# Kernel optimization log

Measured on AMD Instinct MI355X. Metric: run time of the kernel, lower is better.

Reference implementation:

```python
import math
import jax, jax.numpy as jnp
import numpy as np

NUM_HEADS = 16

def _rotate_half(t):
    t1, t2 = jnp.split(t, 2, axis=-1)
    return jnp.concatenate([-t2, t1], axis=-1)

def _apply_rope(t, cos, sin):
    # t: [B, H, S, D]; cos/sin: [S, D] broadcast over batch and heads
    c = cos[None, None, :, :]
    s = sin[None, None, :, :]
    return t * c + _rotate_half(t) * s

def setup_inputs() -> dict:
    key = jax.random.key(0)
    k1, k2, k3, k4, k5 = jax.random.split(key, 5)
    B, S, E, D = 4, 2048, 1024, 1024 // NUM_HEADS
    x = jax.random.normal(k1, (B, S, E), dtype=jnp.float32)
    cos = jax.random.uniform(k2, (S, D), dtype=jnp.float32)
    sin = jax.random.uniform(k3, (S, D), dtype=jnp.float32)
    W_qkv = jax.random.normal(k4, (3 * E, E), dtype=jnp.float32) * (1.0 / math.sqrt(E))
    W_out = jax.random.normal(k5, (E, E), dtype=jnp.float32) * (1.0 / math.sqrt(E))
    return {"x": x, "cos": cos, "sin": sin, "W_qkv": W_qkv, "W_out": W_out}

def reference(x, cos, sin, W_qkv, W_out):
    B, S, E = x.shape
    H = NUM_HEADS
    D = E // H
    # fused QKV projection (torch Linear: y = x @ W^T)
    qkv = jnp.einsum('bse,fe->bsf', x, W_qkv)
    qkv = qkv.reshape(B, S, 3, H, D).transpose(2, 0, 3, 1, 4)  # [3, B, H, S, D]
    q, k, v = qkv[0], qkv[1], qkv[2]
    q = _apply_rope(q, cos, sin)
    k = _apply_rope(k, cos, sin)
    # naive fp32 attention: full [B,H,S,S] score matrix, stable softmax
    scale = 1.0 / math.sqrt(D)
    qf = q.astype(jnp.float32)
    kf = k.astype(jnp.float32)
    vf = v.astype(jnp.float32)
    scores = jnp.einsum('bhqd,bhkd->bhqk', qf, kf) * scale
    attn = jax.nn.softmax(scores, axis=-1)
    o = jnp.einsum('bhqk,bhkd->bhqd', attn, vf).astype(x.dtype)
    o = o.transpose(0, 2, 1, 3).reshape(B, S, E)
    return jnp.einsum('bse,fe->bsf', o, W_out)
```

## Files before the change

kernel.cpp:

```cpp
#include <hip/hip_runtime.h>
#include <hip/hip_bf16.h>

using bf16 = __hip_bfloat16;
typedef __attribute__((ext_vector_type(4))) float f32x4;
typedef __attribute__((ext_vector_type(16))) float f32x16;
typedef short s16x8 __attribute__((ext_vector_type(8)));
typedef unsigned short u16x8 __attribute__((ext_vector_type(8)));

__device__ __forceinline__ unsigned short f2b(float f) {
  bf16 h = __float2bfloat16(f);
  return __builtin_bit_cast(unsigned short, h);
}
__device__ __forceinline__ unsigned cvt_pk_bf16(float lo, float hi) {
  unsigned r;
  asm volatile("v_cvt_pk_bf16_f32 %0, %1, %2" : "=v"(r) : "v"(lo), "v"(hi));
  return r;
}
__device__ __forceinline__ void pl32_swap(unsigned& a, unsigned& b) {
  asm volatile("v_permlane32_swap_b32 %0, %1" : "+v"(a), "+v"(b));
}
__device__ __forceinline__ float fast_exp2(float x) {
#if __has_builtin(__builtin_amdgcn_exp2f)
  return __builtin_amdgcn_exp2f(x);
#else
  return exp2f(x);
#endif
}

__device__ __forceinline__ void async_copy16(const void* g, void* lds) {
  __builtin_amdgcn_global_load_lds(
      (const __attribute__((address_space(1))) void*)g,
      (__attribute__((address_space(3))) void*)lds, 16, 0, 0);
}

__global__ __launch_bounds__(256) void cvt_f32_to_bf16(const float* __restrict__ in,
                                                       ushort* __restrict__ out) {
  long i = ((long)blockIdx.x * 256 + threadIdx.x) * 8;
  float4 a = *(const float4*)(in + i);
  float4 b = *(const float4*)(in + i + 4);
  u16x8 o;
  o[0] = f2b(a.x); o[1] = f2b(a.y); o[2] = f2b(a.z); o[3] = f2b(a.w);
  o[4] = f2b(b.x); o[5] = f2b(b.y); o[6] = f2b(b.z); o[7] = f2b(b.w);
  *(u16x8*)(out + i) = o;
}

__global__ __launch_bounds__(256) void transpose_v(const bf16* __restrict__ qkv,
                                                   ushort* __restrict__ vtg) {
  const int pair = blockIdx.y;
  const int b = pair >> 4, h = pair & 15;
  const int st = blockIdx.x * 64;
  const int tid = threadIdx.x;
  __shared__ ushort T[64][68];
  const ushort* src = (const ushort*)qkv + (long)(b * 2048 + st) * 3072 + 2048 + h * 64;
#pragma unroll
  for (int i = 0; i < 4; ++i) {
    int c2 = tid + i * 256;
    int row = c2 >> 4;
    int d4 = (c2 & 15) * 4;
    *(ushort4*)&T[row][d4] = *(const ushort4*)(src + (long)row * 3072 + d4);
  }
  __syncthreads();
#pragma unroll
  for (int i = 0; i < 4; ++i) {
    int c2 = tid + i * 256;
    int d = c2 >> 4;
    int s4 = (c2 & 15) * 4;
    ushort4 w;
    w.x = T[s4][d]; w.y = T[s4 + 1][d]; w.z = T[s4 + 2][d]; w.w = T[s4 + 3][d];
    *(ushort4*)(vtg + (long)pair * 131072 + (long)d * 2048 + st + s4) = w;
  }
}

__device__ __forceinline__ void storeC(float* p, float v) { *p = v; }
__device__ __forceinline__ void storeC(bf16* p, float v) { *p = __float2bfloat16(v); }

template <typename CT, bool ROPE>
__global__ __launch_bounds__(256) void gemm_bt(const bf16* __restrict__ A,
                                               const bf16* __restrict__ B,
                                               CT* __restrict__ C,
                                               int M, int N, int K,
                                               const float* __restrict__ cosT,
                                               const float* __restrict__ sinT) {
  __shared__ bf16 As[2][128 * 64];
  __shared__ bf16 Bs[2][128 * 64];
  const int tid = threadIdx.x;
  const int lane = tid & 63;
  const int wid = tid >> 6;

  const int nwg = gridDim.x * gridDim.y;
  const int orig = blockIdx.y * gridDim.x + blockIdx.x;
  const int wgid = (orig & 7) * (nwg >> 3) + (orig >> 3);
  const int bx = wgid % gridDim.x;
  const int by = wgid / gridDim.x;

  const int tm = by * 128;
  const int tn = bx * 128;
  const int wr = wid >> 1, wc = wid & 1;
  const int srow = tid >> 3;
  const int scolb = (tid & 7) * 16;
  const int sscolb = scolb ^ ((srow & 7) << 4);

  f32x4 acc[4][4] = {};

  const bf16* Abase = A + (long)(tm + srow) * K + (sscolb >> 1);
  const bf16* Bbase = B + (long)(tn + srow) * K + (sscolb >> 1);

  const int lr = lane & 15;
  const int g = lane >> 4;
  const int sw = (lr & 7) << 4;

  auto stage = [&](int k0, int bb) {
#pragma unroll
    for (int i = 0; i < 4; ++i) {
      async_copy16(Abase + (long)i * 32 * K + k0, (char*)As[bb] + wid * 1024 + i * 4096);
      async_copy16(Bbase + (long)i * 32 * K + k0, (char*)Bs[bb] + wid * 1024 + i * 4096);
    }
  };

  const int nk = K >> 6;
  stage(0, 0);
  stage(64, 1);

  for (int kt = 0; kt < nk; ++kt) {
    const int cur = kt & 1;
    if (kt + 1 < nk) asm volatile("s_waitcnt vmcnt(8)" ::: "memory");
    else             asm volatile("s_waitcnt vmcnt(0)" ::: "memory");
    __builtin_amdgcn_s_barrier();
    __builtin_amdgcn_sched_barrier(0);

#pragma unroll
    for (int ks = 0; ks < 2; ++ks) {
      s16x8 af[4], bff[4];
#pragma unroll
      for (int m = 0; m < 4; ++m) {
        int row = wr * 64 + m * 16 + lr;
        af[m] = *(const s16x8*)((const char*)&As[cur][0] + row * 128 +
                                ((ks * 64 + g * 16) ^ sw));
      }
#pragma unroll
      for (int n = 0; n < 4; ++n) {
        int row = wc * 64 + n * 16 + lr;
        bff[n] = *(const s16x8*)((const char*)&Bs[cur][0] + row * 128 +
                                 ((ks * 64 + g * 16) ^ sw));
      }
#pragma unroll
      for (int m = 0; m < 4; ++m)
#pragma unroll
        for (int n = 0; n < 4; ++n)
          acc[m][n] = __builtin_amdgcn_mfma_f32_16x16x32_bf16(af[m], bff[n], acc[m][n], 0, 0, 0);
    }

    __builtin_amdgcn_s_barrier();
    __builtin_amdgcn_sched_barrier(0);
    if (kt + 2 < nk) stage((kt + 2) << 6, cur);
  }

  const int cc = lane & 15;
  const int cr = (lane >> 4) * 4;
  const int wcol = tn + wc * 64;

  if (ROPE && wcol < 2048) {
    const float sc = (wcol < 1024) ? 0.18033688011112042f : 1.0f;
#pragma unroll
    for (int m = 0; m < 4; ++m)
#pragma unroll
      for (int n = 0; n < 2; ++n) {
        long row0 = tm + wr * 64 + m * 16 + cr;
        long col = wcol + n * 16 + cc;
        int d = n * 16 + cc;
#pragma unroll
        for (int r = 0; r < 4; ++r) {
          int s = (int)((row0 + r) & 2047);
          float lo = acc[m][n][r], hi = acc[m][n + 2][r];
          float c0 = cosT[s * 64 + d], s0v = sinT[s * 64 + d];
          float c1 = cosT[s * 64 + d + 32], s1v = sinT[s * 64 + d + 32];
          storeC(&C[(row0 + r) * (long)N + col], (lo * c0 - hi * s0v) * sc);
          storeC(&C[(row0 + r) * (long)N + col + 32], (hi * c1 + lo * s1v) * sc);
        }
      }
  } else {
#pragma unroll
    for (int m = 0; m < 4; ++m)
#pragma unroll
      for (int n = 0; n < 4; ++n) {
        long row0 = tm + wr * 64 + m * 16 + cr;
        long col = wcol + n * 16 + cc;
#pragma unroll
        for (int r = 0; r < 4; ++r)
          storeC(&C[(row0 + r) * (long)N + col], acc[m][n][r]);
      }
  }
}

__global__ __launch_bounds__(256, 4) void attn_kernel(const bf16* __restrict__ qkv,
                                                      const ushort* __restrict__ vtg,
                                                      ushort* __restrict__ o) {
  const int bid = blockIdx.x;
  const int xcd = bid & 7;
  const int w = bid >> 3;
  const int pair = xcd * 8 + (w >> 4);
  const int qtile = w & 15;
  const int b = pair >> 4, h = pair & 15;
  const int q0 = qtile * 128;
  const int tid = threadIdx.x, lane = tid & 63, wid = tid >> 6;

  const bf16* Qb = qkv + (long)b * 2048 * 3072 + h * 64;
  const bf16* Kb = Qb + 1024;
  const ushort* Vg = vtg + (long)pair * 131072;

  __shared__ bf16 Ks[2][64 * 64];
  __shared__ bf16 Vs[2][64 * 64];

  const int ql = lane & 31;
  const int hi = lane >> 5;
  const int sw = (ql & 7) << 4;

  s16x8 qa[4];
  {
    const bf16* qrow = Qb + (long)(q0 + wid * 32 + ql) * 3072 + hi * 8;
#pragma unroll
    for (int ds = 0; ds < 4; ++ds)
      qa[ds] = *(const s16x8*)(qrow + ds * 16);
  }

  f32x16 oacc[2] = {};
  float lrow = 0.f;

  auto stage = [&](int kt, int bb) {
#pragma unroll
    for (int i = 0; i < 2; ++i) {
      int c = tid + i * 256;
      int row = c >> 3;
      int colb = (c & 7) * 16;
      int scolb = colb ^ ((row & 7) << 4);
      async_copy16(Kb + (long)(kt * 64 + row) * 3072 + (scolb >> 1),
                   (char*)Ks + bb * 8192 + wid * 1024 + i * 4096);
      async_copy16(Vg + (long)row * 2048 + kt * 64 + (scolb >> 1),
                   (char*)Vs + bb * 8192 + wid * 1024 + i * 4096);
    }
  };

  stage(0, 0);
  __syncthreads();

  int cur = 0;
  for (int kt = 0; kt < 32; ++kt) {
    if (kt < 31) stage(kt + 1, cur ^ 1);

    f32x16 sacc[2] = {};
    __builtin_amdgcn_s_setprio(1);
#pragma unroll
    for (int kb = 0; kb < 2; ++kb) {
      const char* krow = (const char*)Ks + cur * 8192 + (kb * 32 + ql) * 128;
#pragma unroll
      for (int ds = 0; ds < 4; ++ds) {
        s16x8 kf = *(const s16x8*)(krow + ((ds * 32 + hi * 16) ^ sw));
        sacc[kb] = __builtin_amdgcn_mfma_f32_32x32x16_bf16(kf, qa[ds], sacc[kb], 0, 0, 0);
      }
    }
    __builtin_amdgcn_s_setprio(0);

    float pv[32];
#pragma unroll
    for (int r = 0; r < 16; ++r) {
      pv[r] = fast_exp2(sacc[0][r]);
      pv[16 + r] = fast_exp2(sacc[1][r]);
    }
    float s16a[16];
#pragma unroll
    for (int i = 0; i < 16; ++i) s16a[i] = pv[i] + pv[i + 16];
#pragma unroll
    for (int i = 0; i < 8; ++i) s16a[i] += s16a[i + 8];
#pragma unroll
    for (int i = 0; i < 4; ++i) s16a[i] += s16a[i + 4];
    float psum = (s16a[0] + s16a[1]) + (s16a[2] + s16a[3]);
    psum += __shfl_xor(psum, 32, 64);
    lrow += psum;

    s16x8 pa[4];
#pragma unroll
    for (int s = 0; s < 4; ++s) {
      unsigned a0 = cvt_pk_bf16(pv[s * 8 + 0], pv[s * 8 + 1]);
      unsigned a1 = cvt_pk_bf16(pv[s * 8 + 2], pv[s * 8 + 3]);
      unsigned b0 = cvt_pk_bf16(pv[s * 8 + 4], pv[s * 8 + 5]);
      unsigned b1 = cvt_pk_bf16(pv[s * 8 + 6], pv[s * 8 + 7]);
      pl32_swap(a0, b0);
      pl32_swap(a1, b1);
      uint4 u{a0, a1, b0, b1};
      pa[s] = __builtin_bit_cast(s16x8, u);
    }

    __builtin_amdgcn_s_setprio(1);
#pragma unroll
    for (int dblk = 0; dblk < 2; ++dblk) {
      const char* vrow = (const char*)Vs + cur * 8192 + (dblk * 32 + ql) * 128;
#pragma unroll
      for (int s = 0; s < 4; ++s) {
        s16x8 vf = *(const s16x8*)(vrow + ((s * 32 + hi * 16) ^ sw));
        oacc[dblk] = __builtin_amdgcn_mfma_f32_32x32x16_bf16(pa[s], vf, oacc[dblk], 0, 0, 0);
      }
    }
    __builtin_amdgcn_s_setprio(0);

    __syncthreads();
    cur ^= 1;
  }

  float linv = 1.f / lrow;
#pragma unroll
  for (int r = 0; r < 16; ++r) {
    int qr = (r & 3) + 8 * (r >> 2) + 4 * hi;
    float inv = __shfl(linv, qr, 64);
    long srow = q0 + wid * 32 + qr;
    ushort* orow = o + ((long)b * 2048 + srow) * 1024 + h * 64 + ql;
    orow[0]  = f2b(oacc[0][r] * inv);
    orow[32] = f2b(oacc[1][r] * inv);
  }
}

extern "C" void kernel_launch(void* const* d_in, const int* in_sizes, int n_in,
                              void* d_out, int out_size, void* d_ws, size_t ws_size,
                              hipStream_t stream) {
  const float* x    = (const float*)d_in[0];
  const float* cosT = (const float*)d_in[1];
  const float* sinT = (const float*)d_in[2];
  const float* Wqkv = (const float*)d_in[3];
  const float* Wout = (const float*)d_in[4];
  float* out = (float*)d_out;

  char* p = (char*)d_ws;
  bf16* xb    = (bf16*)p; p += (size_t)8192 * 1024 * 2;
  bf16* wqkvb = (bf16*)p; p += (size_t)3072 * 1024 * 2;
  bf16* woutb = (bf16*)p; p += (size_t)1024 * 1024 * 2;
  bf16* qkvb  = (bf16*)p; p += (size_t)8192 * 3072 * 2;
  bf16* ob    = (bf16*)p;
  ushort* vtg = (ushort*)xb;

  cvt_f32_to_bf16<<<4096, 256, 0, stream>>>(x, (ushort*)xb);
  cvt_f32_to_bf16<<<1536, 256, 0, stream>>>(Wqkv, (ushort*)wqkvb);
  cvt_f32_to_bf16<<<512, 256, 0, stream>>>(Wout, (ushort*)woutb);

  gemm_bt<bf16, true><<<dim3(24, 64), 256, 0, stream>>>(xb, wqkvb, qkvb, 8192, 3072, 1024,
                                                        cosT, sinT);

  transpose_v<<<dim3(32, 64), 256, 0, stream>>>(qkvb, vtg);

  attn_kernel<<<1024, 256, 0, stream>>>(qkvb, vtg, (ushort*)ob);

  gemm_bt<float, false><<<dim3(8, 64), 256, 0, stream>>>(ob, woutb, out, 8192, 1024, 1024,
                                                         nullptr, nullptr);
}
```

Before: 185.9 us.

## Switch GEMM to register-staged single LDS buffer and merge conversion kernels

Replaces the double-buffered async global-to-LDS copy pipeline in the GEMM with register prefetch of the next tile into a single LDS buffer. Halving LDS allows up to four blocks per CU, which is meant to raise occupancy and hide memory latency. The cost is an extra VGPR round trip and two barriers per k-step. The three fp32-to-bf16 conversion launches are also merged into one kernel to save launch overhead.

```diff
diff --git a/kernel.cpp b/kernel.cpp
--- a/kernel.cpp
+++ b/kernel.cpp
@@ -33,15 +33,22 @@
       (__attribute__((address_space(3))) void*)lds, 16, 0, 0);
 }
 
-__global__ __launch_bounds__(256) void cvt_f32_to_bf16(const float* __restrict__ in,
-                                                       ushort* __restrict__ out) {
-  long i = ((long)blockIdx.x * 256 + threadIdx.x) * 8;
-  float4 a = *(const float4*)(in + i);
-  float4 b = *(const float4*)(in + i + 4);
+__global__ __launch_bounds__(256) void cvt_all(const float* __restrict__ x,
+                                               const float* __restrict__ wqkv,
+                                               const float* __restrict__ wout,
+                                               ushort* __restrict__ out) {
+  long c = (long)blockIdx.x * 256 + threadIdx.x;
+  const float* src;
+  long off;
+  if (c < 1048576)      { src = x;    off = c; }
+  else if (c < 1441792) { src = wqkv; off = c - 1048576; }
+  else                  { src = wout; off = c - 1441792; }
+  float4 a = *(const float4*)(src + off * 8);
+  float4 b = *(const float4*)(src + off * 8 + 4);
   u16x8 o;
   o[0] = f2b(a.x); o[1] = f2b(a.y); o[2] = f2b(a.z); o[3] = f2b(a.w);
   o[4] = f2b(b.x); o[5] = f2b(b.y); o[6] = f2b(b.z); o[7] = f2b(b.w);
-  *(u16x8*)(out + i) = o;
+  *(u16x8*)(out + c * 8) = o;
 }
 
 __global__ __launch_bounds__(256) void transpose_v(const bf16* __restrict__ qkv,
@@ -75,14 +82,14 @@
 __device__ __forceinline__ void storeC(bf16* p, float v) { *p = __float2bfloat16(v); }
 
 template <typename CT, bool ROPE>
-__global__ __launch_bounds__(256) void gemm_bt(const bf16* __restrict__ A,
-                                               const bf16* __restrict__ B,
-                                               CT* __restrict__ C,
-                                               int M, int N, int K,
-                                               const float* __restrict__ cosT,
-                                               const float* __restrict__ sinT) {
-  __shared__ bf16 As[2][128 * 64];
-  __shared__ bf16 Bs[2][128 * 64];
+__global__ __launch_bounds__(256, 4) void gemm_bt(const bf16* __restrict__ A,
+                                                  const bf16* __restrict__ B,
+                                                  CT* __restrict__ C,
+                                                  int M, int N, int K,
+                                                  const float* __restrict__ cosT,
+                                                  const float* __restrict__ sinT) {
+  __shared__ bf16 As[128 * 64];
+  __shared__ bf16 Bs[128 * 64];
   const int tid = threadIdx.x;
   const int lane = tid & 63;
   const int wid = tid >> 6;
@@ -98,35 +105,40 @@
   const int wr = wid >> 1, wc = wid & 1;
   const int srow = tid >> 3;
   const int scolb = (tid & 7) * 16;
-  const int sscolb = scolb ^ ((srow & 7) << 4);
+  const int kdst = srow * 128 + (scolb ^ ((srow & 7) << 4));
 
   f32x4 acc[4][4] = {};
 
-  const bf16* Abase = A + (long)(tm + srow) * K + (sscolb >> 1);
-  const bf16* Bbase = B + (long)(tn + srow) * K + (sscolb >> 1);
+  const bf16* Abase = A + (long)(tm + srow) * K + (scolb >> 1);
+  const bf16* Bbase = B + (long)(tn + srow) * K + (scolb >> 1);
 
   const int lr = lane & 15;
   const int g = lane >> 4;
   const int sw = (lr & 7) << 4;
 
-  auto stage = [&](int k0, int bb) {
+  int4 ra[4], rb[4];
+  auto load = [&](int k0) {
 #pragma unroll
     for (int i = 0; i < 4; ++i) {
-      async_copy16(Abase + (long)i * 32 * K + k0, (char*)As[bb] + wid * 1024 + i * 4096);
-      async_copy16(Bbase + (long)i * 32 * K + k0, (char*)Bs[bb] + wid * 1024 + i * 4096);
+      ra[i] = *(const int4*)(Abase + (long)i * 32 * K + k0);
+      rb[i] = *(const int4*)(Bbase + (long)i * 32 * K + k0);
     }
   };
+  auto write = [&]() {
+#pragma unroll
+    for (int i = 0; i < 4; ++i) {
+      *(int4*)((char*)As + kdst + i * 4096) = ra[i];
+      *(int4*)((char*)Bs + kdst + i * 4096) = rb[i];
+    }
+  };
 
   const int nk = K >> 6;
-  stage(0, 0);
-  stage(64, 1);
+  load(0);
+  write();
+  __syncthreads();
 
   for (int kt = 0; kt < nk; ++kt) {
-    const int cur = kt & 1;
-    if (kt + 1 < nk) asm volatile("s_waitcnt vmcnt(8)" ::: "memory");
-    else             asm volatile("s_waitcnt vmcnt(0)" ::: "memory");
-    __builtin_amdgcn_s_barrier();
-    __builtin_amdgcn_sched_barrier(0);
+    if (kt + 1 < nk) load((kt + 1) << 6);
 
 #pragma unroll
     for (int ks = 0; ks < 2; ++ks) {
@@ -134,13 +146,13 @@
 #pragma unroll
       for (int m = 0; m < 4; ++m) {
         int row = wr * 64 + m * 16 + lr;
-        af[m] = *(const s16x8*)((const char*)&As[cur][0] + row * 128 +
+        af[m] = *(const s16x8*)((const char*)As + row * 128 +
                                 ((ks * 64 + g * 16) ^ sw));
       }
 #pragma unroll
       for (int n = 0; n < 4; ++n) {
         int row = wc * 64 + n * 16 + lr;
-        bff[n] = *(const s16x8*)((const char*)&Bs[cur][0] + row * 128 +
+        bff[n] = *(const s16x8*)((const char*)Bs + row * 128 +
                                  ((ks * 64 + g * 16) ^ sw));
       }
 #pragma unroll
@@ -150,9 +162,11 @@
           acc[m][n] = __builtin_amdgcn_mfma_f32_16x16x32_bf16(af[m], bff[n], acc[m][n], 0, 0, 0);
     }
 
-    __builtin_amdgcn_s_barrier();
-    __builtin_amdgcn_sched_barrier(0);
-    if (kt + 2 < nk) stage((kt + 2) << 6, cur);
+    __syncthreads();
+    if (kt + 1 < nk) {
+      write();
+      __syncthreads();
+    }
   }
 
   const int cc = lane & 15;
@@ -336,9 +350,7 @@
   bf16* ob    = (bf16*)p;
   ushort* vtg = (ushort*)xb;
 
-  cvt_f32_to_bf16<<<4096, 256, 0, stream>>>(x, (ushort*)xb);
-  cvt_f32_to_bf16<<<1536, 256, 0, stream>>>(Wqkv, (ushort*)wqkvb);
-  cvt_f32_to_bf16<<<512, 256, 0, stream>>>(Wout, (ushort*)woutb);
+  cvt_all<<<6144, 256, 0, stream>>>(x, Wqkv, Wout, (ushort*)xb);
 
   gemm_bt<bf16, true><<<dim3(24, 64), 256, 0, stream>>>(xb, wqkvb, qkvb, 8192, 3072, 1024,
                                                         cosT, sinT);
```

Result: slower. 429.3 us (+131.0%).
